# Kernel tuning notes

Hardware: AMD Instinct MI355X
Metric: run time of the kernel (lower is better)

The kernel has to match this reference:

```python
import jax, jax.numpy as jnp
import numpy as np

D = 1024
H = 16
DK = D // H
MLP = 4096
EPS = 1e-5


def layernorm(x, w, b):
    mu = jnp.mean(x, axis=-1, keepdims=True)
    var = jnp.mean(jnp.square(x - mu), axis=-1, keepdims=True)
    return (x - mu) * jax.lax.rsqrt(var + EPS) * w + b


def setup_inputs() -> dict:
    key = jax.random.key(0)
    ks = jax.random.split(key, 12)
    s = 0.02
    return {
        "x": jax.random.normal(ks[0], (8, 1024, D), dtype=jnp.float32),
        "ln1_w": jnp.ones((D,), jnp.float32),
        "ln1_b": jnp.zeros((D,), jnp.float32),
        "wq": jax.random.normal(ks[1], (D, D), jnp.float32) * s,
        "bq": jnp.zeros((D,), jnp.float32),
        "wk": jax.random.normal(ks[2], (D, D), jnp.float32) * s,
        "bk": jnp.zeros((D,), jnp.float32),
        "wv": jax.random.normal(ks[3], (D, D), jnp.float32) * s,
        "bv": jnp.zeros((D,), jnp.float32),
        "wo": jax.random.normal(ks[4], (D, D), jnp.float32) * s,
        "bo": jnp.zeros((D,), jnp.float32),
        "ln2_w": jnp.ones((D,), jnp.float32),
        "ln2_b": jnp.zeros((D,), jnp.float32),
        "w1": jax.random.normal(ks[5], (D, MLP), jnp.float32) * s,
        "b1": jnp.zeros((MLP,), jnp.float32),
        "w2": jax.random.normal(ks[6], (MLP, D), jnp.float32) * s,
        "b2": jnp.zeros((D,), jnp.float32),
    }


def reference(x, ln1_w, ln1_b, wq, bq, wk, bk, wv, bv, wo, bo, ln2_w, ln2_b, w1, b1, w2, b2):
    B, S, _ = x.shape
    h = layernorm(x, ln1_w, ln1_b)
    # QKV projections, split heads: [B, H, S, DK]
    q = (h @ wq + bq).reshape(B, S, H, DK).transpose(0, 2, 1, 3)
    k = (h @ wk + bk).reshape(B, S, H, DK).transpose(0, 2, 1, 3)
    v = (h @ wv + bv).reshape(B, S, H, DK).transpose(0, 2, 1, 3)
    scores = jnp.einsum('bhqd,bhkd->bhqk', q, k) / np.sqrt(DK).astype(np.float32)
    attn = jax.nn.softmax(scores, axis=-1)
    ctx = jnp.einsum('bhqk,bhkd->bhqd', attn, v)
    ctx = ctx.transpose(0, 2, 1, 3).reshape(B, S, D)
    # NOTE: original MultiHeadAttention applies ReLU after the output projection
    attn_out = jax.nn.relu(ctx @ wo + bo)
    out1 = x + attn_out  # dropout is identity in eval
    h2 = layernorm(out1, ln2_w, ln2_b)
    ff = jax.nn.gelu(h2 @ w1 + b1, approximate=False) @ w2 + b2
    return out1 + ff
```

## Files before the change

kernel.cpp:

```cpp
#include <hip/hip_runtime.h>
#include <hip/hip_bf16.h>
#include <math.h>

typedef __bf16 bf16x8 __attribute__((ext_vector_type(8)));
typedef __bf16 bf16x4 __attribute__((ext_vector_type(4)));
typedef float f32x4 __attribute__((ext_vector_type(4)));

typedef __attribute__((address_space(3))) unsigned int lds_u32_t;
typedef __attribute__((address_space(1))) const unsigned int glb_u32_t;

static __device__ __forceinline__ f32x4 mfma16(bf16x8 a, bf16x8 b, f32x4 c) {
  return __builtin_amdgcn_mfma_f32_16x16x32_bf16(a, b, c, 0, 0, 0);
}

static __device__ __forceinline__ float fast_exp2(float x) {
#if __has_builtin(__builtin_amdgcn_exp2f)
  return __builtin_amdgcn_exp2f(x);
#else
  return exp2f(x);
#endif
}

static __device__ __forceinline__ void load_lds16(const __bf16* g, __bf16* l) {
  __builtin_amdgcn_global_load_lds((glb_u32_t*)g, (lds_u32_t*)l, 16, 0, 0);
}

__global__ __launch_bounds__(256) void transpose_w(const float* __restrict__ src,
                                                   __bf16* __restrict__ dst,
                                                   int R, int C) {
  __shared__ float tile[32][33];
  int tx = threadIdx.x, ty = threadIdx.y;
  int c0 = blockIdx.x * 32, r0 = blockIdx.y * 32;
#pragma unroll
  for (int i = 0; i < 4; i++)
    tile[ty + 8 * i][tx] = src[(size_t)(r0 + ty + 8 * i) * C + c0 + tx];
  __syncthreads();
#pragma unroll
  for (int i = 0; i < 4; i++)
    dst[(size_t)(c0 + ty + 8 * i) * R + r0 + tx] = (__bf16)tile[tx][ty + 8 * i];
}

__global__ __launch_bounds__(256) void ln_kernel(const float* __restrict__ x,
                                                 const float* __restrict__ w,
                                                 const float* __restrict__ b,
                                                 __bf16* __restrict__ out) {
  int row = blockIdx.x, tid = threadIdx.x;
  const float* xr = x + (size_t)row * 1024;
  float v[4];
  float s = 0.f, sq = 0.f;
#pragma unroll
  for (int i = 0; i < 4; i++) {
    v[i] = xr[tid + 256 * i];
    s += v[i];
    sq += v[i] * v[i];
  }
#pragma unroll
  for (int off = 1; off < 64; off <<= 1) {
    s += __shfl_xor(s, off, 64);
    sq += __shfl_xor(sq, off, 64);
  }
  __shared__ float red[8];
  int wave = tid >> 6, lane = tid & 63;
  if (lane == 0) { red[wave] = s; red[4 + wave] = sq; }
  __syncthreads();
  if (tid == 0) {
    float S = red[0] + red[1] + red[2] + red[3];
    float SQ = red[4] + red[5] + red[6] + red[7];
    float mu = S * (1.f / 1024.f);
    float var = SQ * (1.f / 1024.f) - mu * mu;
    red[0] = mu;
    red[1] = rsqrtf(var + 1e-5f);
  }
  __syncthreads();
  float mu = red[0], rstd = red[1];
  __bf16* orow = out + (size_t)row * 1024;
#pragma unroll
  for (int i = 0; i < 4; i++) {
    int c = tid + 256 * i;
    orow[c] = (__bf16)((v[i] - mu) * rstd * w[c] + b[c]);
  }
}

enum { MODE_QKV = 0, MODE_WO = 3, MODE_F1 = 4, MODE_F2 = 5 };

template <int MODE>
__global__ __launch_bounds__(256, 2) void gemm_bt(const __bf16* __restrict__ A,
                                                  const __bf16* __restrict__ Bt,
                                                  const float* __restrict__ b0,
                                                  const float* __restrict__ b1,
                                                  const float* __restrict__ b2,
                                                  const float* __restrict__ aux,
                                                  void* __restrict__ o0,
                                                  void* __restrict__ o1,
                                                  void* __restrict__ o2,
                                                  int N, int K) {
  __shared__ __align__(16) __bf16 As[128 * 64];
  __shared__ __align__(16) __bf16 Bs[128 * 64];
  const int tid = threadIdx.x;
  const int m0 = blockIdx.y * 128, n0 = blockIdx.x * 128;
  const int wave = tid >> 6, lane = tid & 63, quad = lane >> 4, l16 = lane & 15;
  const int wm = (wave >> 1) * 64, wn = (wave & 1) * 64;

  int srow[4], sgran[4];
#pragma unroll
  for (int i = 0; i < 4; i++) {
    int inst = wave * 4 + i;
    srow[i] = inst * 8 + (lane >> 3);
    sgran[i] = (lane & 7) ^ (srow[i] & 7);
  }

  const f32x4 zero4 = {0.f, 0.f, 0.f, 0.f};
  f32x4 acc[4][4];
#pragma unroll
  for (int i = 0; i < 4; i++)
#pragma unroll
    for (int j = 0; j < 4; j++) acc[i][j] = zero4;

  for (int kt = 0; kt < K; kt += 64) {
#pragma unroll
    for (int i = 0; i < 4; i++) {
      int inst = wave * 4 + i;
      load_lds16(&A[(size_t)(m0 + srow[i]) * K + kt + sgran[i] * 8], &As[inst * 512]);
      load_lds16(&Bt[(size_t)(n0 + srow[i]) * K + kt + sgran[i] * 8], &Bs[inst * 512]);
    }
    __syncthreads();
#pragma unroll
    for (int ks = 0; ks < 64; ks += 32) {
      bf16x8 af[4], bfv[4];
#pragma unroll
      for (int mi = 0; mi < 4; mi++) {
        int row = wm + 16 * mi + l16;
        int pg = ((ks >> 3) + quad) ^ (row & 7);
        af[mi] = *(const bf16x8*)&As[row * 64 + pg * 8];
      }
#pragma unroll
      for (int ni = 0; ni < 4; ni++) {
        int row = wn + 16 * ni + l16;
        int pg = ((ks >> 3) + quad) ^ (row & 7);
        bfv[ni] = *(const bf16x8*)&Bs[row * 64 + pg * 8];
      }
#pragma unroll
      for (int mi = 0; mi < 4; mi++)
#pragma unroll
        for (int ni = 0; ni < 4; ni++)
          acc[mi][ni] = mfma16(af[mi], bfv[ni], acc[mi][ni]);
    }
    __syncthreads();
  }

  int seg = (n0 >> 10);
  const float* bsel = (MODE == MODE_QKV) ? (seg == 0 ? b0 : seg == 1 ? b1 : b2) : b0;

#pragma unroll
  for (int mi = 0; mi < 4; mi++) {
#pragma unroll
    for (int ni = 0; ni < 4; ni++) {
      int ncol = n0 + wn + 16 * ni + l16;
      int cc = ncol & 1023;
      float bval = bsel[(MODE == MODE_QKV) ? cc : ncol];
#pragma unroll
      for (int r = 0; r < 4; r++) {
        int m = m0 + wm + 16 * mi + quad * 4 + r;
        float val = acc[mi][ni][r] + bval;
        if constexpr (MODE == MODE_QKV) {
          int bb = m >> 10, s = m & 1023, h = cc >> 6, dk = cc & 63;
          if (seg == 0)
            ((__bf16*)o0)[(((size_t)(bb * 16 + h)) * 1024 + s) * 64 + dk] =
                (__bf16)(val * 0.18033688011112042f);
          else if (seg == 1)
            ((__bf16*)o1)[(((size_t)(bb * 16 + h)) * 1024 + s) * 64 + dk] = (__bf16)val;
          else
            ((__bf16*)o2)[(((size_t)(bb * 16 + h)) * 64 + dk) * 1024 + s] = (__bf16)val;
        } else if constexpr (MODE == MODE_WO) {
          val = fmaxf(val, 0.f);
          size_t idx = (size_t)m * 1024 + ncol;
          ((float*)o0)[idx] = aux[idx] + val;
        } else if constexpr (MODE == MODE_F1) {
          float g = 0.5f * val * (1.f + erff(val * 0.70710678118654752f));
          ((__bf16*)o0)[(size_t)m * 4096 + ncol] = (__bf16)g;
        } else {
          size_t idx = (size_t)m * 1024 + ncol;
          ((float*)o0)[idx] = aux[idx] + val;
        }
      }
    }
  }
}

template <int MODE>
__global__ __launch_bounds__(512, 2) void gemm256(const __bf16* __restrict__ A,
                                                  const __bf16* __restrict__ Bt,
                                                  const float* __restrict__ b0,
                                                  const float* __restrict__ b1,
                                                  const float* __restrict__ b2,
                                                  const float* __restrict__ aux,
                                                  void* __restrict__ o0,
                                                  void* __restrict__ o1,
                                                  void* __restrict__ o2,
                                                  int N, int K) {
  __shared__ __align__(16) __bf16 As[4][8192];
  __shared__ __align__(16) __bf16 Bs[4][8192];
  const int tid = threadIdx.x;
  const int m0 = blockIdx.y * 256, n0 = blockIdx.x * 256;
  const int wave = tid >> 6, lane = tid & 63, quad = lane >> 4, l16 = lane & 15;
  const int wr = wave >> 2, wc = wave & 3;

  const int Lsub = lane >> 3;
  const int sp = (lane & 7) ^ Lsub;
  const int par = sp & 1, kq = sp >> 1;
  const int rbase = wave * 16 + 2 * Lsub + par;
  const __bf16* pA0 = A + (size_t)(m0 + rbase) * K + 8 * kq;
  const __bf16* pA1 = A + (size_t)(m0 + rbase + 128) * K + 8 * kq;
  const __bf16* pB0 = Bt + (size_t)(n0 + rbase) * K + 8 * kq;
  const __bf16* pB1 = Bt + (size_t)(n0 + rbase + 128) * K + 8 * kq;
  const int dst0 = (wave * 8) * 64;
  const int dst1 = (64 + wave * 8) * 64;

  int afOff[8], bfOff[4];
#pragma unroll
  for (int mi = 0; mi < 8; mi++) {
    int r = wr * 128 + 16 * mi + l16;
    int L = r >> 1;
    int sl = (2 * quad + (r & 1)) ^ (L & 7);
    afOff[mi] = L * 128 + sl * 16;
  }
#pragma unroll
  for (int nj = 0; nj < 4; nj++) {
    int c = wc * 64 + 16 * nj + l16;
    int L = c >> 1;
    int sl = (2 * quad + (c & 1)) ^ (L & 7);
    bfOff[nj] = L * 128 + sl * 16;
  }

  const f32x4 zero4 = {0.f, 0.f, 0.f, 0.f};
  f32x4 acc[8][4];
#pragma unroll
  for (int i = 0; i < 8; i++)
#pragma unroll
    for (int j = 0; j < 4; j++) acc[i][j] = zero4;

  const int nt = K >> 5;

  auto stage = [&](int t) {
    int slot = t & 3;
    __bf16* a = &As[slot][0];
    __bf16* b = &Bs[slot][0];
    load_lds16(pA0, a + dst0);
    load_lds16(pA1, a + dst1);
    load_lds16(pB0, b + dst0);
    load_lds16(pB1, b + dst1);
    pA0 += 32; pA1 += 32; pB0 += 32; pB1 += 32;
  };

  auto window = [&](int t, bool dostage) {
    const char* ab = (const char*)&As[t & 3][0];
    const char* bb = (const char*)&Bs[t & 3][0];
    bf16x8 af[8], bfv[4];
#pragma unroll
    for (int mi = 0; mi < 8; mi++) af[mi] = *(const bf16x8*)(ab + afOff[mi]);
#pragma unroll
    for (int nj = 0; nj < 4; nj++) bfv[nj] = *(const bf16x8*)(bb + bfOff[nj]);
    if (dostage) stage(t + 3);
    __builtin_amdgcn_s_setprio(1);
#pragma unroll
    for (int mi = 0; mi < 8; mi++)
#pragma unroll
      for (int nj = 0; nj < 4; nj++)
        acc[mi][nj] = mfma16(af[mi], bfv[nj], acc[mi][nj]);
    __builtin_amdgcn_s_setprio(0);
  };

  stage(0);
  stage(1);
  stage(2);
  asm volatile("s_waitcnt vmcnt(8)" ::: "memory");
  __builtin_amdgcn_s_barrier();
  __builtin_amdgcn_sched_barrier(0);

  for (int t = 0; t < nt - 3; ++t) {
    window(t, true);
    asm volatile("s_waitcnt vmcnt(8)" ::: "memory");
    __builtin_amdgcn_s_barrier();
    __builtin_amdgcn_sched_barrier(0);
  }
  window(nt - 3, false);
  asm volatile("s_waitcnt vmcnt(4)" ::: "memory");
  __builtin_amdgcn_s_barrier();
  __builtin_amdgcn_sched_barrier(0);
  window(nt - 2, false);
  asm volatile("s_waitcnt vmcnt(0)" ::: "memory");
  __builtin_amdgcn_s_barrier();
  __builtin_amdgcn_sched_barrier(0);
  window(nt - 1, false);

  int seg = (n0 >> 10);
  const float* bsel = (MODE == MODE_QKV) ? (seg == 0 ? b0 : seg == 1 ? b1 : b2) : b0;

#pragma unroll
  for (int mi = 0; mi < 8; mi++) {
#pragma unroll
    for (int nj = 0; nj < 4; nj++) {
      int ncol = n0 + wc * 64 + 16 * nj + l16;
      int cc = ncol & 1023;
      float bval = bsel[(MODE == MODE_QKV) ? cc : ncol];
#pragma unroll
      for (int r = 0; r < 4; r++) {
        int m = m0 + wr * 128 + 16 * mi + quad * 4 + r;
        float val = acc[mi][nj][r] + bval;
        if constexpr (MODE == MODE_QKV) {
          int bb = m >> 10, s = m & 1023, h = cc >> 6, dk = cc & 63;
          if (seg == 0)
            ((__bf16*)o0)[(((size_t)(bb * 16 + h)) * 1024 + s) * 64 + dk] =
                (__bf16)(val * 0.18033688011112042f);
          else if (seg == 1)
            ((__bf16*)o1)[(((size_t)(bb * 16 + h)) * 1024 + s) * 64 + dk] = (__bf16)val;
          else
            ((__bf16*)o2)[(((size_t)(bb * 16 + h)) * 64 + dk) * 1024 + s] = (__bf16)val;
        } else if constexpr (MODE == MODE_WO) {
          val = fmaxf(val, 0.f);
          size_t idx = (size_t)m * 1024 + ncol;
          ((float*)o0)[idx] = aux[idx] + val;
        } else if constexpr (MODE == MODE_F1) {
          float g = 0.5f * val * (1.f + erff(val * 0.70710678118654752f));
          ((__bf16*)o0)[(size_t)m * 4096 + ncol] = (__bf16)g;
        } else {
          size_t idx = (size_t)m * 1024 + ncol;
          ((float*)o0)[idx] = aux[idx] + val;
        }
      }
    }
  }
}

__global__ __launch_bounds__(256, 2) void attn_kernel(const __bf16* __restrict__ Q,
                                                      const __bf16* __restrict__ Kp,
                                                      const __bf16* __restrict__ Vt,
                                                      __bf16* __restrict__ ctx) {
  __shared__ __align__(16) __bf16 Ks[2][64][64];
  __shared__ __align__(16) __bf16 Vs[2][64][64];
  __shared__ __align__(16) __bf16 Ps[2][4][32][72];
  const int tid = threadIdx.x;
  const int bh = blockIdx.x, qb = blockIdx.y;
  const int wave = tid >> 6, lane = tid & 63, quad = lane >> 4, l16 = lane & 15;
  const int qrow0 = qb * 128 + wave * 32;

  bf16x8 aq[2][2];
#pragma unroll
  for (int mi = 0; mi < 2; mi++) {
    const __bf16* qrow = Q + ((size_t)bh * 1024 + qrow0 + mi * 16 + l16) * 64;
    aq[mi][0] = *(const bf16x8*)&qrow[8 * quad];
    aq[mi][1] = *(const bf16x8*)&qrow[32 + 8 * quad];
  }

  const f32x4 zero4 = {0.f, 0.f, 0.f, 0.f};
  f32x4 o[2][4];
  float lp[2] = {0.f, 0.f};
#pragma unroll
  for (int mi = 0; mi < 2; mi++)
#pragma unroll
    for (int nj = 0; nj < 4; nj++) o[mi][nj] = zero4;

  const __bf16* kb0 = Kp + (size_t)bh * 65536;
  const __bf16* vb0 = Vt + (size_t)bh * 65536;

  const int srow = lane >> 3;
  const int sgran = (lane & 7) ^ srow;
  const int r0 = wave * 16;

  auto stage = [&](int t) {
    int buf = t & 1;
    const __bf16* ks = kb0 + (size_t)(t * 64 + r0 + srow) * 64 + sgran * 8;
    load_lds16(ks, &Ks[buf][r0][0]);
    load_lds16(ks + 8 * 64, &Ks[buf][r0 + 8][0]);
    const __bf16* vs = vb0 + (size_t)(r0 + srow) * 1024 + t * 64 + sgran * 8;
    load_lds16(vs, &Vs[buf][r0][0]);
    load_lds16(vs + 8 * 1024, &Vs[buf][r0 + 8][0]);
  };

  int kOff[4][2], vOff[4][2];
#pragma unroll
  for (int ni = 0; ni < 4; ni++) {
    int r = 16 * ni + l16;
#pragma unroll
    for (int half = 0; half < 2; half++) {
      int g = quad + 4 * half;
      kOff[ni][half] = r * 128 + ((g ^ (r & 7)) * 16);
      vOff[ni][half] = kOff[ni][half];
    }
  }

  stage(0);
  asm volatile("s_waitcnt vmcnt(0)" ::: "memory");
  __builtin_amdgcn_s_barrier();

  for (int t = 0; t < 16; ++t) {
    const int buf = t & 1;
    if (t < 15) stage(t + 1);
    const char* kbuf_ = (const char*)&Ks[buf][0][0];
    const char* vbuf_ = (const char*)&Vs[buf][0][0];
    bf16x8 kf[4][2];
#pragma unroll
    for (int ni = 0; ni < 4; ni++) {
      kf[ni][0] = *(const bf16x8*)(kbuf_ + kOff[ni][0]);
      kf[ni][1] = *(const bf16x8*)(kbuf_ + kOff[ni][1]);
    }
    f32x4 st[2][4];
    __builtin_amdgcn_s_setprio(1);
#pragma unroll
    for (int mi = 0; mi < 2; mi++)
#pragma unroll
      for (int ni = 0; ni < 4; ni++) {
        st[mi][ni] = mfma16(kf[ni][0], aq[mi][0], zero4);
        st[mi][ni] = mfma16(kf[ni][1], aq[mi][1], st[mi][ni]);
      }
    __builtin_amdgcn_s_setprio(0);
    bf16x8 vf[2][4];
#pragma unroll
    for (int nj = 0; nj < 4; nj++) {
      vf[0][nj] = *(const bf16x8*)(vbuf_ + vOff[nj][0]);
      vf[1][nj] = *(const bf16x8*)(vbuf_ + vOff[nj][1]);
    }
#pragma unroll
    for (int mi = 0; mi < 2; mi++)
#pragma unroll
      for (int ni = 0; ni < 4; ni++) {
        union { bf16x4 v4; __bf16 b[4]; } pk;
#pragma unroll
        for (int r = 0; r < 4; r++) {
          float p = fast_exp2(st[mi][ni][r]);
          lp[mi] += p;
          pk.b[r] = (__bf16)p;
        }
        *(bf16x4*)&Ps[buf][wave][16 * mi + l16][16 * ni + 4 * quad] = pk.v4;
      }
    bf16x8 pa[2][2];
#pragma unroll
    for (int mi = 0; mi < 2; mi++) {
      pa[mi][0] = *(const bf16x8*)&Ps[buf][wave][16 * mi + l16][8 * quad];
      pa[mi][1] = *(const bf16x8*)&Ps[buf][wave][16 * mi + l16][32 + 8 * quad];
    }
    __builtin_amdgcn_s_setprio(1);
#pragma unroll
    for (int mi = 0; mi < 2; mi++)
#pragma unroll
      for (int nj = 0; nj < 4; nj++) {
        o[mi][nj] = mfma16(pa[mi][0], vf[0][nj], o[mi][nj]);
        o[mi][nj] = mfma16(pa[mi][1], vf[1][nj], o[mi][nj]);
      }
    __builtin_amdgcn_s_setprio(0);
    if (t < 15) {
      asm volatile("s_waitcnt vmcnt(0)" ::: "memory");
      __builtin_amdgcn_s_barrier();
    }
  }

#pragma unroll
  for (int mi = 0; mi < 2; mi++) {
    lp[mi] += __shfl_xor(lp[mi], 16, 64);
    lp[mi] += __shfl_xor(lp[mi], 32, 64);
  }

  int bb = bh >> 4, h = bh & 15;
#pragma unroll
  for (int mi = 0; mi < 2; mi++)
#pragma unroll
    for (int r = 0; r < 4; r++) {
      float inv = 1.f / __shfl(lp[mi], 4 * quad + r, 64);
      int s = qrow0 + mi * 16 + 4 * quad + r;
#pragma unroll
      for (int nj = 0; nj < 4; nj++)
        ctx[((size_t)(bb * 1024 + s)) * 1024 + h * 64 + nj * 16 + l16] =
            (__bf16)(o[mi][nj][r] * inv);
    }
}

extern "C" void kernel_launch(void* const* d_in, const int* in_sizes, int n_in,
                              void* d_out, int out_size, void* d_ws, size_t ws_size,
                              hipStream_t stream) {
  const float* x = (const float*)d_in[0];
  const float* ln1w = (const float*)d_in[1];
  const float* ln1b = (const float*)d_in[2];
  const float* wq = (const float*)d_in[3];
  const float* bq = (const float*)d_in[4];
  const float* wk = (const float*)d_in[5];
  const float* bk = (const float*)d_in[6];
  const float* wv = (const float*)d_in[7];
  const float* bv = (const float*)d_in[8];
  const float* wo = (const float*)d_in[9];
  const float* bo = (const float*)d_in[10];
  const float* ln2w = (const float*)d_in[11];
  const float* ln2b = (const float*)d_in[12];
  const float* w1 = (const float*)d_in[13];
  const float* b1 = (const float*)d_in[14];
  const float* w2 = (const float*)d_in[15];
  const float* b2 = (const float*)d_in[16];
  float* out = (float*)d_out;

  char* ws = (char*)d_ws;
  const size_t MB = 1024 * 1024;
  __bf16* wqkv_t = (__bf16*)(ws + 0 * MB);
  __bf16* wq_t = (__bf16*)(ws + 0 * MB);
  __bf16* wk_t = (__bf16*)(ws + 2 * MB);
  __bf16* wv_t = (__bf16*)(ws + 4 * MB);
  __bf16* wo_t = (__bf16*)(ws + 6 * MB);
  __bf16* w1_t = (__bf16*)(ws + 8 * MB);
  __bf16* w2_t = (__bf16*)(ws + 16 * MB);
  __bf16* hbuf = (__bf16*)(ws + 24 * MB);
  __bf16* qbuf = (__bf16*)(ws + 40 * MB);
  __bf16* kbuf = (__bf16*)(ws + 56 * MB);
  __bf16* vtbuf = (__bf16*)(ws + 72 * MB);
  __bf16* ctxbuf = (__bf16*)(ws + 88 * MB);
  __bf16* ff1 = (__bf16*)(ws + 40 * MB);

  dim3 tb(32, 8);
  transpose_w<<<dim3(32, 32), tb, 0, stream>>>(wq, wq_t, 1024, 1024);
  transpose_w<<<dim3(32, 32), tb, 0, stream>>>(wk, wk_t, 1024, 1024);
  transpose_w<<<dim3(32, 32), tb, 0, stream>>>(wv, wv_t, 1024, 1024);
  transpose_w<<<dim3(32, 32), tb, 0, stream>>>(wo, wo_t, 1024, 1024);
  transpose_w<<<dim3(128, 32), tb, 0, stream>>>(w1, w1_t, 1024, 4096);
  transpose_w<<<dim3(32, 128), tb, 0, stream>>>(w2, w2_t, 4096, 1024);

  ln_kernel<<<8192, 256, 0, stream>>>(x, ln1w, ln1b, hbuf);

  gemm256<MODE_QKV><<<dim3(12, 32), 512, 0, stream>>>(
      hbuf, wqkv_t, bq, bk, bv, nullptr, qbuf, kbuf, vtbuf, 3072, 1024);

  attn_kernel<<<dim3(128, 8), 256, 0, stream>>>(qbuf, kbuf, vtbuf, ctxbuf);

  gemm_bt<MODE_WO><<<dim3(8, 64), 256, 0, stream>>>(
      ctxbuf, wo_t, bo, nullptr, nullptr, x, out, nullptr, nullptr, 1024, 1024);

  ln_kernel<<<8192, 256, 0, stream>>>(out, ln2w, ln2b, hbuf);

  gemm256<MODE_F1><<<dim3(16, 32), 512, 0, stream>>>(
      hbuf, w1_t, b1, nullptr, nullptr, nullptr, ff1, nullptr, nullptr, 4096, 1024);
  gemm_bt<MODE_F2><<<dim3(8, 64), 256, 0, stream>>>(
      ff1, w2_t, b2, nullptr, nullptr, out, out, nullptr, nullptr, 1024, 4096);
}
```

Before: 528.8 us.

## Use k-major LDS layout in gemm256 and a fast erf-based GELU

The GELU epilogue replaces erff with an Abramowitz-Stegun polynomial built on hardware rcp and exp2, cutting transcendental cost in the F1 GEMM epilogue. The 256x256 GEMM staging changes so that each wave loads 64 whole rows (A for waves 0-3, B for waves 4-7). Rows are stored in a k-major (quad-split) LDS layout, which removes the XOR swizzle and precomputed offset tables. The new fragment reads are simple strided addresses, but the unswizzled layout may create LDS bank conflicts, and the GELU approximation adds about 1e-7 absolute error.

```diff
diff --git a/kernel.cpp b/kernel.cpp
--- a/kernel.cpp
+++ b/kernel.cpp
@@ -19,6 +19,26 @@
 #else
   return exp2f(x);
 #endif
+}
+
+static __device__ __forceinline__ float fast_rcp(float x) {
+#if __has_builtin(__builtin_amdgcn_rcpf)
+  return __builtin_amdgcn_rcpf(x);
+#else
+  return 1.f / x;
+#endif
+}
+
+static __device__ __forceinline__ float fast_gelu(float x) {
+  float z = x * 0.70710678118654752f;
+  float az = fabsf(z);
+  float t = fast_rcp(fmaf(0.3275911f, az, 1.f));
+  float poly = t * fmaf(t, fmaf(t, fmaf(t, fmaf(t, 1.061405429f, -1.453152027f),
+                                        1.421413741f), -0.284496736f), 0.254829592f);
+  float e = fast_exp2(-az * az * 1.4426950408889634f);
+  float erf_abs = fmaf(-poly, e, 1.f);
+  float erfv = copysignf(erf_abs, z);
+  return 0.5f * x * (1.f + erfv);
 }
 
 static __device__ __forceinline__ void load_lds16(const __bf16* g, __bf16* l) {
@@ -176,8 +196,7 @@
           size_t idx = (size_t)m * 1024 + ncol;
           ((float*)o0)[idx] = aux[idx] + val;
         } else if constexpr (MODE == MODE_F1) {
-          float g = 0.5f * val * (1.f + erff(val * 0.70710678118654752f));
-          ((__bf16*)o0)[(size_t)m * 4096 + ncol] = (__bf16)g;
+          ((__bf16*)o0)[(size_t)m * 4096 + ncol] = (__bf16)fast_gelu(val);
         } else {
           size_t idx = (size_t)m * 1024 + ncol;
           ((float*)o0)[idx] = aux[idx] + val;
@@ -205,32 +224,13 @@
   const int wave = tid >> 6, lane = tid & 63, quad = lane >> 4, l16 = lane & 15;
   const int wr = wave >> 2, wc = wave & 3;
 
-  const int Lsub = lane >> 3;
-  const int sp = (lane & 7) ^ Lsub;
-  const int par = sp & 1, kq = sp >> 1;
-  const int rbase = wave * 16 + 2 * Lsub + par;
-  const __bf16* pA0 = A + (size_t)(m0 + rbase) * K + 8 * kq;
-  const __bf16* pA1 = A + (size_t)(m0 + rbase + 128) * K + 8 * kq;
-  const __bf16* pB0 = Bt + (size_t)(n0 + rbase) * K + 8 * kq;
-  const __bf16* pB1 = Bt + (size_t)(n0 + rbase + 128) * K + 8 * kq;
-  const int dst0 = (wave * 8) * 64;
-  const int dst1 = (64 + wave * 8) * 64;
-
-  int afOff[8], bfOff[4];
-#pragma unroll
-  for (int mi = 0; mi < 8; mi++) {
-    int r = wr * 128 + 16 * mi + l16;
-    int L = r >> 1;
-    int sl = (2 * quad + (r & 1)) ^ (L & 7);
-    afOff[mi] = L * 128 + sl * 16;
-  }
-#pragma unroll
-  for (int nj = 0; nj < 4; nj++) {
-    int c = wc * 64 + 16 * nj + l16;
-    int L = c >> 1;
-    int sl = (2 * quad + (c & 1)) ^ (L & 7);
-    bfOff[nj] = L * 128 + sl * 16;
-  }
+  const __bf16* pS = (wave < 4)
+                         ? A + (size_t)(m0 + wave * 64 + lane) * K
+                         : Bt + (size_t)(n0 + (wave - 4) * 64 + lane) * K;
+  const int dstoff = (wave & 3) * 512;
+
+  const int aoff = quad * 4096 + (wr * 128 + l16) * 16;
+  const int boff = quad * 4096 + (wc * 64 + l16) * 16;
 
   const f32x4 zero4 = {0.f, 0.f, 0.f, 0.f};
   f32x4 acc[8][4];
@@ -242,14 +242,10 @@
   const int nt = K >> 5;
 
   auto stage = [&](int t) {
-    int slot = t & 3;
-    __bf16* a = &As[slot][0];
-    __bf16* b = &Bs[slot][0];
-    load_lds16(pA0, a + dst0);
-    load_lds16(pA1, a + dst1);
-    load_lds16(pB0, b + dst0);
-    load_lds16(pB1, b + dst1);
-    pA0 += 32; pA1 += 32; pB0 += 32; pB1 += 32;
+    __bf16* b = ((wave < 4) ? &As[t & 3][0] : &Bs[t & 3][0]) + dstoff;
+#pragma unroll
+    for (int g = 0; g < 4; g++) load_lds16(pS + 8 * g, b + 2048 * g);
+    pS += 32;
   };
 
   auto window = [&](int t, bool dostage) {
@@ -257,9 +253,9 @@
     const char* bb = (const char*)&Bs[t & 3][0];
     bf16x8 af[8], bfv[4];
 #pragma unroll
-    for (int mi = 0; mi < 8; mi++) af[mi] = *(const bf16x8*)(ab + afOff[mi]);
-#pragma unroll
-    for (int nj = 0; nj < 4; nj++) bfv[nj] = *(const bf16x8*)(bb + bfOff[nj]);
+    for (int mi = 0; mi < 8; mi++) af[mi] = *(const bf16x8*)(ab + aoff + mi * 256);
+#pragma unroll
+    for (int nj = 0; nj < 4; nj++) bfv[nj] = *(const bf16x8*)(bb + boff + nj * 256);
     if (dostage) stage(t + 3);
     __builtin_amdgcn_s_setprio(1);
 #pragma unroll
@@ -321,8 +317,7 @@
           size_t idx = (size_t)m * 1024 + ncol;
           ((float*)o0)[idx] = aux[idx] + val;
         } else if constexpr (MODE == MODE_F1) {
-          float g = 0.5f * val * (1.f + erff(val * 0.70710678118654752f));
-          ((__bf16*)o0)[(size_t)m * 4096 + ncol] = (__bf16)g;
+          ((__bf16*)o0)[(size_t)m * 4096 + ncol] = (__bf16)fast_gelu(val);
         } else {
           size_t idx = (size_t)m * 1024 + ncol;
           ((float*)o0)[idx] = aux[idx] + val;
```

Measured after the change: 545.3 us. 1.03x slower.
